# Kernel optimization log

Hardware: AMD Instinct MI355X
Metric: run time of the kernel (lower is better)

The kernel has to match this reference:

```python
import jax, jax.numpy as jnp
import numpy as np
from jax import lax

NUM_HEADS = 8  # init_kwargs: num_heads
TOPK = 7       # hard-coded in DMF.forward


def setup_inputs() -> dict:
    key = jax.random.key(0)
    k1, k2, k3, k4 = jax.random.split(key, 4)
    b, dim, H, W = 8, 384, 128, 128
    x = jax.random.normal(k1, (b, dim, H, W), dtype=jnp.float32)
    qkv_w = jax.random.normal(k2, (dim * 3, dim), dtype=jnp.float32) * 0.05   # 1x1 conv weight
    dw_w = jax.random.normal(k3, (dim * 3, 1, 3, 3), dtype=jnp.float32) * 0.05  # depthwise 3x3
    proj_w = jax.random.normal(k4, (dim, dim), dtype=jnp.float32) * 0.05     # 1x1 conv weight
    temperature = jnp.ones((NUM_HEADS, 1, 1), dtype=jnp.float32)
    return {"x": x, "qkv_w": qkv_w, "dw_w": dw_w, "proj_w": proj_w, "temperature": temperature}


def _l2norm(t, eps=1e-12):
    # matches torch.nn.functional.normalize(dim=-1)
    n = jnp.sqrt(jnp.sum(t * t, axis=-1, keepdims=True))
    return t / jnp.maximum(n, eps)


def reference(x, qkv_w, dw_w, proj_w, temperature):
    b, c, h, w = x.shape
    ch = c // NUM_HEADS  # channels per head

    # 1x1 conv (pointwise) -> depthwise 3x3 conv
    qkv = jnp.einsum('bchw,oc->bohw', x, qkv_w)
    qkv = lax.conv_general_dilated(
        qkv, dw_w, window_strides=(1, 1), padding=[(1, 1), (1, 1)],
        feature_group_count=qkv.shape[1],
        dimension_numbers=('NCHW', 'OIHW', 'NCHW'))
    q, k, v = jnp.split(qkv, 3, axis=1)

    def to_heads(t):  # b (head ch) h w -> b head ch (h w)
        return t.reshape(b, NUM_HEADS, ch, h * w)

    q = _l2norm(to_heads(q))
    k = _l2norm(to_heads(k))
    v = to_heads(v)

    # channel attention: [b, head, ch, ch]
    attn_weight = jnp.einsum('bhcn,bhdn->bhcd', q, k) * temperature

    # top-k sparsify along last dim, then masked softmax
    _, idx = lax.top_k(attn_weight, TOPK)                      # [b,h,ch,TOPK]
    cols = jnp.arange(attn_weight.shape[-1])
    mask = (idx[..., None] == cols).any(axis=-2)               # [b,h,ch,ch] bool
    attn = jnp.where(mask, attn_weight, -jnp.inf)
    attn = jax.nn.softmax(attn, axis=-1)

    out = jnp.einsum('bhcd,bhdn->bhcn', attn, v).reshape(b, c, h, w)
    out = jnp.einsum('bchw,oc->bohw', out, proj_w)
    return out
```

## Files before the change

kernel.cpp:

```cpp
#include <hip/hip_runtime.h>

#define HWN 16384
#define WDIM 128

typedef __bf16 bf16x8 __attribute__((ext_vector_type(8)));
typedef float floatx4 __attribute__((ext_vector_type(4)));

#define LSTR 36

__global__ __launch_bounds__(256, 2) void gemm_mfma3(
    const __bf16* __restrict__ Ah, const __bf16* __restrict__ Al,
    const float* __restrict__ B, float* __restrict__ C,
    int K, long sA, long sB, long sC) {
  __shared__ __bf16 sAh[128 * LSTR], sAl[128 * LSTR], sBh[128 * LSTR], sBl[128 * LSTR];
  const int bz = blockIdx.z;
  Ah += (long)bz * sA;
  Al += (long)bz * sA;
  B += (long)bz * sB;
  C += (long)bz * sC;
  const int tid = threadIdx.x;
  const int n0 = blockIdx.x << 7, m0 = blockIdx.y << 7;
  const int arow = tid >> 1, akq = (tid & 1) << 4;
  const int bn = (tid & 63) << 1;
  const int bkb = (tid >> 6) << 3;
  const int lane = tid & 63, wv = tid >> 6;
  const int mq = (wv & 1) << 6, nq = (wv >> 1) << 6;
  const int fm = lane & 15, fq = lane >> 4;
  floatx4 acc[4][4] = {};
  for (int k0 = 0; k0 < K; k0 += 32) {
    const __bf16* pAh = Ah + (long)(m0 + arow) * K + k0 + akq;
    const __bf16* pAl = Al + (long)(m0 + arow) * K + k0 + akq;
    bf16x8 a0 = *(const bf16x8*)pAh;
    bf16x8 a1 = *(const bf16x8*)(pAh + 8);
    bf16x8 a2 = *(const bf16x8*)pAl;
    bf16x8 a3 = *(const bf16x8*)(pAl + 8);
    const float* pB = B + (long)(k0 + bkb) * HWN + n0 + bn;
    float2 v[8];
#pragma unroll
    for (int r = 0; r < 8; ++r) v[r] = *(const float2*)(pB + (long)r * HWN);
    bf16x8 bh0, bh1, bl0, bl1;
#pragma unroll
    for (int r = 0; r < 8; ++r) {
      float vx = v[r].x, vy = v[r].y;
      __bf16 hx = (__bf16)vx, hy = (__bf16)vy;
      bh0[r] = hx;
      bh1[r] = hy;
      bl0[r] = (__bf16)(vx - (float)hx);
      bl1[r] = (__bf16)(vy - (float)hy);
    }
    __syncthreads();
    *(bf16x8*)&sAh[arow * LSTR + akq] = a0;
    *(bf16x8*)&sAh[arow * LSTR + akq + 8] = a1;
    *(bf16x8*)&sAl[arow * LSTR + akq] = a2;
    *(bf16x8*)&sAl[arow * LSTR + akq + 8] = a3;
    *(bf16x8*)&sBh[bn * LSTR + bkb] = bh0;
    *(bf16x8*)&sBh[(bn + 1) * LSTR + bkb] = bh1;
    *(bf16x8*)&sBl[bn * LSTR + bkb] = bl0;
    *(bf16x8*)&sBl[(bn + 1) * LSTR + bkb] = bl1;
    __syncthreads();
    bf16x8 fAh[4], fAl[4];
#pragma unroll
    for (int i = 0; i < 4; ++i) {
      fAh[i] = *(const bf16x8*)&sAh[(mq + i * 16 + fm) * LSTR + fq * 8];
      fAl[i] = *(const bf16x8*)&sAl[(mq + i * 16 + fm) * LSTR + fq * 8];
    }
#pragma unroll
    for (int j = 0; j < 4; ++j) {
      bf16x8 bh = *(const bf16x8*)&sBh[(nq + j * 16 + fm) * LSTR + fq * 8];
      bf16x8 bl = *(const bf16x8*)&sBl[(nq + j * 16 + fm) * LSTR + fq * 8];
#pragma unroll
      for (int i = 0; i < 4; ++i) {
        acc[i][j] = __builtin_amdgcn_mfma_f32_16x16x32_bf16(fAh[i], bh, acc[i][j], 0, 0, 0);
        acc[i][j] = __builtin_amdgcn_mfma_f32_16x16x32_bf16(fAl[i], bh, acc[i][j], 0, 0, 0);
        acc[i][j] = __builtin_amdgcn_mfma_f32_16x16x32_bf16(fAh[i], bl, acc[i][j], 0, 0, 0);
      }
    }
  }
#pragma unroll
  for (int i = 0; i < 4; ++i)
#pragma unroll
    for (int j = 0; j < 4; ++j) {
      const int col = n0 + nq + j * 16 + fm;
#pragma unroll
      for (int r = 0; r < 4; ++r) {
        const int row = m0 + mq + i * 16 + fq * 4 + r;
        C[(long)row * HWN + col] = acc[i][j][r];
      }
    }
}

__global__ __launch_bounds__(256) void split_w(
    const float* __restrict__ w, __bf16* __restrict__ hi, __bf16* __restrict__ lo, int n) {
  int i = blockIdx.x * 256 + threadIdx.x;
  if (i < n) {
    float v = w[i];
    __bf16 h = (__bf16)v;
    hi[i] = h;
    lo[i] = (__bf16)(v - (float)h);
  }
}

__global__ __launch_bounds__(256) void dw_all3(
    const float* __restrict__ qkv1, const float* __restrict__ dww,
    float* __restrict__ dwout, float* __restrict__ qs, float* __restrict__ ks, int b0) {
  const int tid = threadIdx.x;
  const int ch = blockIdx.x;
  const int yh = blockIdx.y;
  const int bz = blockIdx.z;
  const int xg = tid & 31;
  const int rg = tid >> 5;
  const float4* P = (const float4*)(qkv1 + ((long)bz * 1152 + ch) * HWN);
  float4* O = (float4*)(dwout + ((long)bz * 1152 + ch) * HWN);
  const float* wp = dww + (long)ch * 9;
  const float w00 = wp[0], w01 = wp[1], w02 = wp[2];
  const float w10 = wp[3], w11 = wp[4], w12 = wp[5];
  const float w20 = wp[6], w21 = wp[7], w22 = wp[8];
  const int y0 = (yh << 6) + (rg << 3);

  float4 vr[10];
#pragma unroll
  for (int r = 0; r < 10; ++r) {
    int yy = y0 - 1 + r;
    vr[r] = make_float4(0.f, 0.f, 0.f, 0.f);
    if (yy >= 0 && yy < WDIM) vr[r] = P[yy * 32 + xg];
  }
  float lf[10], rt[10];
#pragma unroll
  for (int r = 0; r < 10; ++r) {
    float l_ = __shfl_up(vr[r].w, 1, 64);
    float r_ = __shfl_down(vr[r].x, 1, 64);
    lf[r] = (xg == 0) ? 0.f : l_;
    rt[r] = (xg == 31) ? 0.f : r_;
  }
  float sq = 0.f;
#pragma unroll
  for (int i = 0; i < 8; ++i) {
    const float t0 = lf[i], t1 = vr[i].x, t2 = vr[i].y, t3 = vr[i].z, t4 = vr[i].w, t5 = rt[i];
    const float m0_ = lf[i + 1], m1 = vr[i + 1].x, m2 = vr[i + 1].y, m3 = vr[i + 1].z,
                m4 = vr[i + 1].w, m5 = rt[i + 1];
    const float b0_ = lf[i + 2], b1 = vr[i + 2].x, b2 = vr[i + 2].y, b3 = vr[i + 2].z,
                b4 = vr[i + 2].w, b5 = rt[i + 2];
    float o0 = w00 * t0 + w01 * t1 + w02 * t2 + w10 * m0_ + w11 * m1 + w12 * m2 +
               w20 * b0_ + w21 * b1 + w22 * b2;
    float o1 = w00 * t1 + w01 * t2 + w02 * t3 + w10 * m1 + w11 * m2 + w12 * m3 +
               w20 * b1 + w21 * b2 + w22 * b3;
    float o2 = w00 * t2 + w01 * t3 + w02 * t4 + w10 * m2 + w11 * m3 + w12 * m4 +
               w20 * b2 + w21 * b3 + w22 * b4;
    float o3 = w00 * t3 + w01 * t4 + w02 * t5 + w10 * m3 + w11 * m4 + w12 * m5 +
               w20 * b3 + w21 * b4 + w22 * b5;
    sq += o0 * o0 + o1 * o1 + o2 * o2 + o3 * o3;
    O[(y0 + i) * 32 + xg] = make_float4(o0, o1, o2, o3);
  }

  if (ch < 768) {
#pragma unroll
    for (int off = 32; off >= 1; off >>= 1) sq += __shfl_down(sq, off, 64);
    if ((tid & 63) == 0) {
      int b = b0 + bz;
      if (ch < 384)
        atomicAdd(qs + b * 384 + ch, sq);
      else
        atomicAdd(ks + b * 384 + (ch - 384), sq);
    }
  }
}

#define GPAD 132
__global__ __launch_bounds__(256) void gram256(
    const float* __restrict__ dwout, float* __restrict__ gram, int b0) {
  __shared__ float qt[48 * GPAD];
  __shared__ float kt[48 * GPAD];
  const int tid = threadIdx.x;
  const int kc = blockIdx.x;
  const int h = blockIdx.y;
  const int bz = blockIdx.z;
  const float* Q = dwout + ((long)bz * 1152 + h * 48) * HWN;
  const float* K = Q + 384L * HWN;
  const int c0 = (tid & 15) * 3;
  const int d0 = (tid >> 4) * 3;
  float g[3][3] = {};
  for (int p0 = kc * 512; p0 < kc * 512 + 512; p0 += 128) {
    __syncthreads();
#pragma unroll
    for (int i = tid; i < 1536; i += 256) {
      int r = i >> 5, x4 = (i & 31) << 2;
      *(float4*)&qt[r * GPAD + x4] = *(const float4*)(Q + (long)r * HWN + p0 + x4);
      *(float4*)&kt[r * GPAD + x4] = *(const float4*)(K + (long)r * HWN + p0 + x4);
    }
    __syncthreads();
#pragma unroll 4
    for (int p = 0; p < 128; p += 4) {
      float4 qv[3], kv[3];
#pragma unroll
      for (int i = 0; i < 3; ++i) qv[i] = *(const float4*)&qt[(c0 + i) * GPAD + p];
#pragma unroll
      for (int j = 0; j < 3; ++j) kv[j] = *(const float4*)&kt[(d0 + j) * GPAD + p];
#pragma unroll
      for (int i = 0; i < 3; ++i)
#pragma unroll
        for (int j = 0; j < 3; ++j)
          g[i][j] += qv[i].x * kv[j].x + qv[i].y * kv[j].y + qv[i].z * kv[j].z +
                     qv[i].w * kv[j].w;
    }
  }
  float* gb = gram + (long)((b0 + bz) * 8 + h) * 2304;
#pragma unroll
  for (int i = 0; i < 3; ++i)
#pragma unroll
    for (int j = 0; j < 3; ++j) atomicAdd(gb + (c0 + i) * 48 + (d0 + j), g[i][j]);
}

__global__ __launch_bounds__(64) void topk_softmax(
    const float* __restrict__ gram, const float* __restrict__ qs, const float* __restrict__ ks,
    const float* __restrict__ temp, float* __restrict__ attn, int b0) {
  const int z = blockIdx.x;
  const int b = b0 + (z >> 3), h = z & 7;
  __shared__ float kn[48];
  const int tid = threadIdx.x;
  if (tid < 48) kn[tid] = fmaxf(sqrtf(ks[b * 384 + h * 48 + tid]), 1e-12f);
  __syncthreads();
  if (tid >= 48) return;
  const int c = tid;
  float qn = fmaxf(sqrtf(qs[b * 384 + h * 48 + c]), 1e-12f);
  float tv = temp[h];
  const float* gr = gram + (long)(b * 8 + h) * 2304 + c * 48;
  float s[48];
#pragma unroll
  for (int d = 0; d < 48; ++d) s[d] = gr[d] / (qn * kn[d]) * tv;
  unsigned long long sel = 0ull;
  float m0 = 0.f;
  for (int it = 0; it < 7; ++it) {
    float mx = -3.0e38f;
    int mi = 0;
#pragma unroll
    for (int d = 0; d < 48; ++d) {
      bool taken = (sel >> d) & 1ull;
      if (!taken && s[d] > mx) { mx = s[d]; mi = d; }
    }
    sel |= (1ull << mi);
    if (it == 0) m0 = mx;
  }
  float sum = 0.f;
  float e[48];
#pragma unroll
  for (int d = 0; d < 48; ++d) {
    bool t = (sel >> d) & 1ull;
    float ev = t ? expf(s[d] - m0) : 0.f;
    e[d] = ev;
    sum += ev;
  }
  float inv = 1.f / sum;
  float* ar = attn + (long)(b * 8 + h) * 2304 + c * 48;
#pragma unroll
  for (int d = 0; d < 48; ++d) ar[d] = e[d] * inv;
}

__global__ __launch_bounds__(256) void build_M(
    const float* __restrict__ attn, const float* __restrict__ pw,
    __bf16* __restrict__ Mh, __bf16* __restrict__ Ml, int b0) {
  const int b = b0 + blockIdx.x;
  const int h = blockIdx.y;
  __shared__ float at[48][49];
  const int tid = threadIdx.x;
  for (int i = tid; i < 2304; i += 256) at[i / 48][i % 48] = attn[(long)(b * 8 + h) * 2304 + i];
  __syncthreads();
  for (int idx = tid; idx < 384 * 48; idx += 256) {
    int o = idx / 48, d = idx % 48;
    const float* pr = pw + (long)o * 384 + h * 48;
    float acc = 0.f;
#pragma unroll
    for (int c = 0; c < 48; ++c) acc += pr[c] * at[c][d];
    long oi = ((long)b * 384 + o) * 384 + h * 48 + d;
    __bf16 hh = (__bf16)acc;
    Mh[oi] = hh;
    Ml[oi] = (__bf16)(acc - (float)hh);
  }
}

extern "C" void kernel_launch(void* const* d_in, const int* in_sizes, int n_in,
                              void* d_out, int out_size, void* d_ws, size_t ws_size,
                              hipStream_t stream) {
  const float* x = (const float*)d_in[0];
  const float* qkv_w = (const float*)d_in[1];
  const float* dw_w = (const float*)d_in[2];
  const float* proj_w = (const float*)d_in[3];
  const float* temp = (const float*)d_in[4];
  float* out = (float*)d_out;
  float* ws = (float*)d_ws;

  float* gram = ws;
  float* qs = gram + 147456;
  float* ks = qs + 3072;
  float* attn = ks + 3072;
  __bf16* Wh = (__bf16*)(attn + 147456);
  __bf16* Wl = Wh + 442368;
  __bf16* Mh = Wl + 442368;
  __bf16* Ml = Mh + 1179648;
  float* qkv1 = (float*)(Ml + 1179648);
  const long SMALLS = 1333248L;
  const long PERB = 37748736L;
  long wsf = (long)(ws_size / 4);
  int nb = (int)((wsf - SMALLS) / PERB);
  if (nb < 1) nb = 1;
  if (nb > 8) nb = 8;
  float* dwout = qkv1 + (long)nb * 18874368L;

  hipMemsetAsync(gram, 0, (147456 + 3072 + 3072) * sizeof(float), stream);
  split_w<<<dim3((442368 + 255) / 256), 256, 0, stream>>>(qkv_w, Wh, Wl, 442368);

  for (int b0 = 0; b0 < 8; b0 += nb) {
    int nbc = (8 - b0 < nb) ? (8 - b0) : nb;
    gemm_mfma3<<<dim3(128, 9, nbc), 256, 0, stream>>>(
        Wh, Wl, x + (long)b0 * 6291456L, qkv1, 384, 0L, 6291456L, 18874368L);
    dw_all3<<<dim3(1152, 2, nbc), 256, 0, stream>>>(qkv1, dw_w, dwout, qs, ks, b0);
    gram256<<<dim3(32, 8, nbc), 256, 0, stream>>>(dwout, gram, b0);
    topk_softmax<<<dim3(nbc * 8), 64, 0, stream>>>(gram, qs, ks, temp, attn, b0);
    build_M<<<dim3(nbc, 8), 256, 0, stream>>>(attn, proj_w, Mh, Ml, b0);
    gemm_mfma3<<<dim3(128, 3, nbc), 256, 0, stream>>>(
        Mh + (long)b0 * 147456L, Ml + (long)b0 * 147456L, dwout + 768L * HWN,
        out + (long)b0 * 6291456L, 384, 147456L, 18874368L, 6291456L);
  }
}
```

Before: 1.412 ms.

## Fuse depthwise conv into gram kernel, store V as split bf16, merge topk with M

The q/k depthwise convolution is now recomputed inside the gram kernel, one image row at a time into shared memory, so the fp32 q/k dwout tensors are never written or read back. A separate kernel applies the conv only to the v channels and stores them pre-split into bf16 hi/lo halves. The final GEMM then reads bf16 B operands directly instead of converting fp32 on load. topk_softmax and build_M are merged into one kernel, and the workspace per batch shrinks so more batches fit per chunk. The cost is extra per-row loads and conv arithmetic inside the gram kernel, plus a gram grid that now loops over rows of the image.

After: 1.679 ms. 18.9% more time.

```diff
diff --git a/kernel.cpp b/kernel.cpp
--- a/kernel.cpp
+++ b/kernel.cpp
@@ -4,6 +4,8 @@
 #define WDIM 128
 
 typedef __bf16 bf16x8 __attribute__((ext_vector_type(8)));
+typedef __bf16 bf16x4 __attribute__((ext_vector_type(4)));
+typedef __bf16 bf16x2 __attribute__((ext_vector_type(2)));
 typedef float floatx4 __attribute__((ext_vector_type(4)));
 
 #define LSTR 36
@@ -89,6 +91,90 @@
     }
 }
 
+__global__ __launch_bounds__(256, 2) void gemm_bf3(
+    const __bf16* __restrict__ Ah, const __bf16* __restrict__ Al,
+    const __bf16* __restrict__ Bh, const __bf16* __restrict__ Bl,
+    float* __restrict__ C, int K, long sA, long sB, long sC) {
+  __shared__ __bf16 sAh[128 * LSTR], sAl[128 * LSTR], sBh[128 * LSTR], sBl[128 * LSTR];
+  const int bz = blockIdx.z;
+  Ah += (long)bz * sA;
+  Al += (long)bz * sA;
+  Bh += (long)bz * sB;
+  Bl += (long)bz * sB;
+  C += (long)bz * sC;
+  const int tid = threadIdx.x;
+  const int n0 = blockIdx.x << 7, m0 = blockIdx.y << 7;
+  const int arow = tid >> 1, akq = (tid & 1) << 4;
+  const int bn = (tid & 63) << 1;
+  const int bkb = (tid >> 6) << 3;
+  const int lane = tid & 63, wv = tid >> 6;
+  const int mq = (wv & 1) << 6, nq = (wv >> 1) << 6;
+  const int fm = lane & 15, fq = lane >> 4;
+  floatx4 acc[4][4] = {};
+  for (int k0 = 0; k0 < K; k0 += 32) {
+    const __bf16* pAh = Ah + (long)(m0 + arow) * K + k0 + akq;
+    const __bf16* pAl = Al + (long)(m0 + arow) * K + k0 + akq;
+    bf16x8 a0 = *(const bf16x8*)pAh;
+    bf16x8 a1 = *(const bf16x8*)(pAh + 8);
+    bf16x8 a2 = *(const bf16x8*)pAl;
+    bf16x8 a3 = *(const bf16x8*)(pAl + 8);
+    const __bf16* pBh = Bh + (long)(k0 + bkb) * HWN + n0 + bn;
+    const __bf16* pBl = Bl + (long)(k0 + bkb) * HWN + n0 + bn;
+    bf16x2 vh[8], vl[8];
+#pragma unroll
+    for (int r = 0; r < 8; ++r) {
+      vh[r] = *(const bf16x2*)(pBh + (long)r * HWN);
+      vl[r] = *(const bf16x2*)(pBl + (long)r * HWN);
+    }
+    bf16x8 bh0, bh1, bl0, bl1;
+#pragma unroll
+    for (int r = 0; r < 8; ++r) {
+      bh0[r] = vh[r][0];
+      bh1[r] = vh[r][1];
+      bl0[r] = vl[r][0];
+      bl1[r] = vl[r][1];
+    }
+    __syncthreads();
+    *(bf16x8*)&sAh[arow * LSTR + akq] = a0;
+    *(bf16x8*)&sAh[arow * LSTR + akq + 8] = a1;
+    *(bf16x8*)&sAl[arow * LSTR + akq] = a2;
+    *(bf16x8*)&sAl[arow * LSTR + akq + 8] = a3;
+    *(bf16x8*)&sBh[bn * LSTR + bkb] = bh0;
+    *(bf16x8*)&sBh[(bn + 1) * LSTR + bkb] = bh1;
+    *(bf16x8*)&sBl[bn * LSTR + bkb] = bl0;
+    *(bf16x8*)&sBl[(bn + 1) * LSTR + bkb] = bl1;
+    __syncthreads();
+    bf16x8 fAh[4], fAl[4];
+#pragma unroll
+    for (int i = 0; i < 4; ++i) {
+      fAh[i] = *(const bf16x8*)&sAh[(mq + i * 16 + fm) * LSTR + fq * 8];
+      fAl[i] = *(const bf16x8*)&sAl[(mq + i * 16 + fm) * LSTR + fq * 8];
+    }
+#pragma unroll
+    for (int j = 0; j < 4; ++j) {
+      bf16x8 bh = *(const bf16x8*)&sBh[(nq + j * 16 + fm) * LSTR + fq * 8];
+      bf16x8 bl = *(const bf16x8*)&sBl[(nq + j * 16 + fm) * LSTR + fq * 8];
+#pragma unroll
+      for (int i = 0; i < 4; ++i) {
+        acc[i][j] = __builtin_amdgcn_mfma_f32_16x16x32_bf16(fAh[i], bh, acc[i][j], 0, 0, 0);
+        acc[i][j] = __builtin_amdgcn_mfma_f32_16x16x32_bf16(fAl[i], bh, acc[i][j], 0, 0, 0);
+        acc[i][j] = __builtin_amdgcn_mfma_f32_16x16x32_bf16(fAh[i], bl, acc[i][j], 0, 0, 0);
+      }
+    }
+  }
+#pragma unroll
+  for (int i = 0; i < 4; ++i)
+#pragma unroll
+    for (int j = 0; j < 4; ++j) {
+      const int col = n0 + nq + j * 16 + fm;
+#pragma unroll
+      for (int r = 0; r < 4; ++r) {
+        const int row = m0 + mq + i * 16 + fq * 4 + r;
+        C[(long)row * HWN + col] = acc[i][j][r];
+      }
+    }
+}
+
 __global__ __launch_bounds__(256) void split_w(
     const float* __restrict__ w, __bf16* __restrict__ hi, __bf16* __restrict__ lo, int n) {
   int i = blockIdx.x * 256 + threadIdx.x;
@@ -100,23 +186,21 @@
   }
 }
 
-__global__ __launch_bounds__(256) void dw_all3(
+__global__ __launch_bounds__(256) void dw_v(
     const float* __restrict__ qkv1, const float* __restrict__ dww,
-    float* __restrict__ dwout, float* __restrict__ qs, float* __restrict__ ks, int b0) {
+    __bf16* __restrict__ Vh, __bf16* __restrict__ Vl) {
   const int tid = threadIdx.x;
   const int ch = blockIdx.x;
   const int yh = blockIdx.y;
   const int bz = blockIdx.z;
   const int xg = tid & 31;
   const int rg = tid >> 5;
-  const float4* P = (const float4*)(qkv1 + ((long)bz * 1152 + ch) * HWN);
-  float4* O = (float4*)(dwout + ((long)bz * 1152 + ch) * HWN);
-  const float* wp = dww + (long)ch * 9;
+  const float4* P = (const float4*)(qkv1 + ((long)bz * 1152 + 768 + ch) * HWN);
+  const float* wp = dww + (long)(768 + ch) * 9;
   const float w00 = wp[0], w01 = wp[1], w02 = wp[2];
   const float w10 = wp[3], w11 = wp[4], w12 = wp[5];
   const float w20 = wp[6], w21 = wp[7], w22 = wp[8];
   const int y0 = (yh << 6) + (rg << 3);
-
   float4 vr[10];
 #pragma unroll
   for (int r = 0; r < 10; ++r) {
@@ -132,7 +216,7 @@
     lf[r] = (xg == 0) ? 0.f : l_;
     rt[r] = (xg == 31) ? 0.f : r_;
   }
-  float sq = 0.f;
+  const long obase = ((long)bz * 384 + ch) * HWN;
 #pragma unroll
   for (int i = 0; i < 8; ++i) {
     const float t0 = lf[i], t1 = vr[i].x, t2 = vr[i].y, t3 = vr[i].z, t4 = vr[i].w, t5 = rt[i];
@@ -148,53 +232,79 @@
                w20 * b2 + w21 * b3 + w22 * b4;
     float o3 = w00 * t3 + w01 * t4 + w02 * t5 + w10 * m3 + w11 * m4 + w12 * m5 +
                w20 * b3 + w21 * b4 + w22 * b5;
-    sq += o0 * o0 + o1 * o1 + o2 * o2 + o3 * o3;
-    O[(y0 + i) * 32 + xg] = make_float4(o0, o1, o2, o3);
-  }
-
-  if (ch < 768) {
-#pragma unroll
-    for (int off = 32; off >= 1; off >>= 1) sq += __shfl_down(sq, off, 64);
-    if ((tid & 63) == 0) {
-      int b = b0 + bz;
-      if (ch < 384)
-        atomicAdd(qs + b * 384 + ch, sq);
-      else
-        atomicAdd(ks + b * 384 + (ch - 384), sq);
-    }
+    bf16x4 h4, l4;
+    __bf16 h0 = (__bf16)o0, h1 = (__bf16)o1, h2 = (__bf16)o2, h3 = (__bf16)o3;
+    h4[0] = h0; h4[1] = h1; h4[2] = h2; h4[3] = h3;
+    l4[0] = (__bf16)(o0 - (float)h0);
+    l4[1] = (__bf16)(o1 - (float)h1);
+    l4[2] = (__bf16)(o2 - (float)h2);
+    l4[3] = (__bf16)(o3 - (float)h3);
+    long off = obase + (y0 + i) * WDIM + xg * 4;
+    *(bf16x4*)&Vh[off] = h4;
+    *(bf16x4*)&Vl[off] = l4;
   }
 }
 
 #define GPAD 132
-__global__ __launch_bounds__(256) void gram256(
-    const float* __restrict__ dwout, float* __restrict__ gram, int b0) {
-  __shared__ float qt[48 * GPAD];
-  __shared__ float kt[48 * GPAD];
+__global__ __launch_bounds__(256) void gram_dw(
+    const float* __restrict__ qkv1, const float* __restrict__ dww,
+    float* __restrict__ gram, float* __restrict__ qs, float* __restrict__ ks, int b0) {
+  __shared__ float dq[48 * GPAD];
+  __shared__ float dk[48 * GPAD];
   const int tid = threadIdx.x;
-  const int kc = blockIdx.x;
+  const int yc = blockIdx.x;
   const int h = blockIdx.y;
   const int bz = blockIdx.z;
-  const float* Q = dwout + ((long)bz * 1152 + h * 48) * HWN;
-  const float* K = Q + 384L * HWN;
+  const int xg = tid & 31;
+  const int grp = tid >> 5;
   const int c0 = (tid & 15) * 3;
   const int d0 = (tid >> 4) * 3;
+  const long bb = (long)bz * 1152;
   float g[3][3] = {};
-  for (int p0 = kc * 512; p0 < kc * 512 + 512; p0 += 128) {
-    __syncthreads();
-#pragma unroll
-    for (int i = tid; i < 1536; i += 256) {
-      int r = i >> 5, x4 = (i & 31) << 2;
-      *(float4*)&qt[r * GPAD + x4] = *(const float4*)(Q + (long)r * HWN + p0 + x4);
-      *(float4*)&kt[r * GPAD + x4] = *(const float4*)(K + (long)r * HWN + p0 + x4);
+  float sq[12] = {};
+  for (int y = yc * 4; y < yc * 4 + 4; ++y) {
+    __syncthreads();
+#pragma unroll
+    for (int gi = 0; gi < 12; ++gi) {
+      const int cl = grp * 12 + gi;
+      const int gch = (cl < 48) ? (h * 48 + cl) : (384 + h * 48 + (cl - 48));
+      const float* sp = qkv1 + (bb + gch) * HWN;
+      const float* wp = dww + (long)gch * 9;
+      float4 r0 = make_float4(0.f, 0.f, 0.f, 0.f);
+      float4 r2 = make_float4(0.f, 0.f, 0.f, 0.f);
+      if (y > 0) r0 = *(const float4*)(sp + (y - 1) * WDIM + xg * 4);
+      float4 r1 = *(const float4*)(sp + y * WDIM + xg * 4);
+      if (y < WDIM - 1) r2 = *(const float4*)(sp + (y + 1) * WDIM + xg * 4);
+      float l0 = __shfl_up(r0.w, 1, 32), l1 = __shfl_up(r1.w, 1, 32), l2 = __shfl_up(r2.w, 1, 32);
+      float q0 = __shfl_down(r0.x, 1, 32), q1 = __shfl_down(r1.x, 1, 32),
+            q2 = __shfl_down(r2.x, 1, 32);
+      if (xg == 0) { l0 = 0.f; l1 = 0.f; l2 = 0.f; }
+      if (xg == 31) { q0 = 0.f; q1 = 0.f; q2 = 0.f; }
+      const float w00 = wp[0], w01 = wp[1], w02 = wp[2];
+      const float w10 = wp[3], w11 = wp[4], w12 = wp[5];
+      const float w20 = wp[6], w21 = wp[7], w22 = wp[8];
+      const float e0[6] = {l0, r0.x, r0.y, r0.z, r0.w, q0};
+      const float e1[6] = {l1, r1.x, r1.y, r1.z, r1.w, q1};
+      const float e2[6] = {l2, r2.x, r2.y, r2.z, r2.w, q2};
+      float o[4];
+#pragma unroll
+      for (int j = 0; j < 4; ++j) {
+        o[j] = w00 * e0[j] + w01 * e0[j + 1] + w02 * e0[j + 2] +
+               w10 * e1[j] + w11 * e1[j + 1] + w12 * e1[j + 2] +
+               w20 * e2[j] + w21 * e2[j + 1] + w22 * e2[j + 2];
+        sq[gi] += o[j] * o[j];
+      }
+      float* dst = (cl < 48) ? &dq[cl * GPAD] : &dk[(cl - 48) * GPAD];
+      *(float4*)&dst[xg * 4] = make_float4(o[0], o[1], o[2], o[3]);
     }
     __syncthreads();
 #pragma unroll 4
     for (int p = 0; p < 128; p += 4) {
       float4 qv[3], kv[3];
 #pragma unroll
-      for (int i = 0; i < 3; ++i) qv[i] = *(const float4*)&qt[(c0 + i) * GPAD + p];
-#pragma unroll
-      for (int j = 0; j < 3; ++j) kv[j] = *(const float4*)&kt[(d0 + j) * GPAD + p];
+      for (int i = 0; i < 3; ++i) qv[i] = *(const float4*)&dq[(c0 + i) * GPAD + p];
+#pragma unroll
+      for (int j = 0; j < 3; ++j) kv[j] = *(const float4*)&dk[(d0 + j) * GPAD + p];
 #pragma unroll
       for (int i = 0; i < 3; ++i)
 #pragma unroll
@@ -203,66 +313,72 @@
                      qv[i].w * kv[j].w;
     }
   }
-  float* gb = gram + (long)((b0 + bz) * 8 + h) * 2304;
+  const int b = b0 + bz;
+#pragma unroll
+  for (int gi = 0; gi < 12; ++gi) {
+    float s = sq[gi];
+#pragma unroll
+    for (int off = 16; off >= 1; off >>= 1) s += __shfl_down(s, off, 32);
+    if (xg == 0) {
+      int cl = grp * 12 + gi;
+      if (cl < 48)
+        atomicAdd(qs + b * 384 + h * 48 + cl, s);
+      else
+        atomicAdd(ks + b * 384 + h * 48 + (cl - 48), s);
+    }
+  }
+  float* gb = gram + (long)(b * 8 + h) * 2304;
 #pragma unroll
   for (int i = 0; i < 3; ++i)
 #pragma unroll
     for (int j = 0; j < 3; ++j) atomicAdd(gb + (c0 + i) * 48 + (d0 + j), g[i][j]);
 }
 
-__global__ __launch_bounds__(64) void topk_softmax(
+__global__ __launch_bounds__(256) void attn_M(
     const float* __restrict__ gram, const float* __restrict__ qs, const float* __restrict__ ks,
-    const float* __restrict__ temp, float* __restrict__ attn, int b0) {
+    const float* __restrict__ temp, const float* __restrict__ pw,
+    __bf16* __restrict__ Mh, __bf16* __restrict__ Ml, int b0) {
   const int z = blockIdx.x;
   const int b = b0 + (z >> 3), h = z & 7;
   __shared__ float kn[48];
+  __shared__ float at[48][49];
   const int tid = threadIdx.x;
   if (tid < 48) kn[tid] = fmaxf(sqrtf(ks[b * 384 + h * 48 + tid]), 1e-12f);
   __syncthreads();
-  if (tid >= 48) return;
-  const int c = tid;
-  float qn = fmaxf(sqrtf(qs[b * 384 + h * 48 + c]), 1e-12f);
-  float tv = temp[h];
-  const float* gr = gram + (long)(b * 8 + h) * 2304 + c * 48;
-  float s[48];
-#pragma unroll
-  for (int d = 0; d < 48; ++d) s[d] = gr[d] / (qn * kn[d]) * tv;
-  unsigned long long sel = 0ull;
-  float m0 = 0.f;
-  for (int it = 0; it < 7; ++it) {
-    float mx = -3.0e38f;
-    int mi = 0;
+  if (tid < 48) {
+    const int c = tid;
+    float qn = fmaxf(sqrtf(qs[b * 384 + h * 48 + c]), 1e-12f);
+    float tv = temp[h];
+    const float* gr = gram + (long)(b * 8 + h) * 2304 + c * 48;
+    float s[48];
+#pragma unroll
+    for (int d = 0; d < 48; ++d) s[d] = gr[d] / (qn * kn[d]) * tv;
+    unsigned long long sel = 0ull;
+    float m0 = 0.f;
+    for (int it = 0; it < 7; ++it) {
+      float mx = -3.0e38f;
+      int mi = 0;
+#pragma unroll
+      for (int d = 0; d < 48; ++d) {
+        bool taken = (sel >> d) & 1ull;
+        if (!taken && s[d] > mx) { mx = s[d]; mi = d; }
+      }
+      sel |= (1ull << mi);
+      if (it == 0) m0 = mx;
+    }
+    float sum = 0.f;
+    float e[48];
 #pragma unroll
     for (int d = 0; d < 48; ++d) {
-      bool taken = (sel >> d) & 1ull;
-      if (!taken && s[d] > mx) { mx = s[d]; mi = d; }
-    }
-    sel |= (1ull << mi);
-    if (it == 0) m0 = mx;
-  }
-  float sum = 0.f;
-  float e[48];
-#pragma unroll
-  for (int d = 0; d < 48; ++d) {
-    bool t = (sel >> d) & 1ull;
-    float ev = t ? expf(s[d] - m0) : 0.f;
-    e[d] = ev;
-    sum += ev;
-  }
-  float inv = 1.f / sum;
-  float* ar = attn + (long)(b * 8 + h) * 2304 + c * 48;
-#pragma unroll
-  for (int d = 0; d < 48; ++d) ar[d] = e[d] * inv;
-}
-
-__global__ __launch_bounds__(256) void build_M(
-    const float* __restrict__ attn, const float* __restrict__ pw,
-    __bf16* __restrict__ Mh, __bf16* __restrict__ Ml, int b0) {
-  const int b = b0 + blockIdx.x;
-  const int h = blockIdx.y;
-  __shared__ float at[48][49];
-  const int tid = threadIdx.x;
-  for (int i = tid; i < 2304; i += 256) at[i / 48][i % 48] = attn[(long)(b * 8 + h) * 2304 + i];
+      bool t = (sel >> d) & 1ull;
+      float ev = t ? expf(s[d] - m0) : 0.f;
+      e[d] = ev;
+      sum += ev;
+    }
+    float inv = 1.f / sum;
+#pragma unroll
+    for (int d = 0; d < 48; ++d) at[c][d] = e[d] * inv;
+  }
   __syncthreads();
   for (int idx = tid; idx < 384 * 48; idx += 256) {
     int o = idx / 48, d = idx % 48;
@@ -291,19 +407,19 @@
   float* gram = ws;
   float* qs = gram + 147456;
   float* ks = qs + 3072;
-  float* attn = ks + 3072;
-  __bf16* Wh = (__bf16*)(attn + 147456);
+  __bf16* Wh = (__bf16*)(ks + 3072);
   __bf16* Wl = Wh + 442368;
   __bf16* Mh = Wl + 442368;
   __bf16* Ml = Mh + 1179648;
   float* qkv1 = (float*)(Ml + 1179648);
-  const long SMALLS = 1333248L;
-  const long PERB = 37748736L;
+  const long SMALLS = 1775616L;
+  const long PERB = 25165824L;
   long wsf = (long)(ws_size / 4);
   int nb = (int)((wsf - SMALLS) / PERB);
   if (nb < 1) nb = 1;
   if (nb > 8) nb = 8;
-  float* dwout = qkv1 + (long)nb * 18874368L;
+  __bf16* Vh = (__bf16*)(qkv1 + (long)nb * 18874368L);
+  __bf16* Vl = Vh + (long)nb * 6291456L;
 
   hipMemsetAsync(gram, 0, (147456 + 3072 + 3072) * sizeof(float), stream);
   split_w<<<dim3((442368 + 255) / 256), 256, 0, stream>>>(qkv_w, Wh, Wl, 442368);
@@ -312,12 +428,11 @@
     int nbc = (8 - b0 < nb) ? (8 - b0) : nb;
     gemm_mfma3<<<dim3(128, 9, nbc), 256, 0, stream>>>(
         Wh, Wl, x + (long)b0 * 6291456L, qkv1, 384, 0L, 6291456L, 18874368L);
-    dw_all3<<<dim3(1152, 2, nbc), 256, 0, stream>>>(qkv1, dw_w, dwout, qs, ks, b0);
-    gram256<<<dim3(32, 8, nbc), 256, 0, stream>>>(dwout, gram, b0);
-    topk_softmax<<<dim3(nbc * 8), 64, 0, stream>>>(gram, qs, ks, temp, attn, b0);
-    build_M<<<dim3(nbc, 8), 256, 0, stream>>>(attn, proj_w, Mh, Ml, b0);
-    gemm_mfma3<<<dim3(128, 3, nbc), 256, 0, stream>>>(
-        Mh + (long)b0 * 147456L, Ml + (long)b0 * 147456L, dwout + 768L * HWN,
-        out + (long)b0 * 6291456L, 384, 147456L, 18874368L, 6291456L);
-  }
-}
+    dw_v<<<dim3(384, 2, nbc), 256, 0, stream>>>(qkv1, dw_w, Vh, Vl);
+    gram_dw<<<dim3(32, 8, nbc), 256, 0, stream>>>(qkv1, dw_w, gram, qs, ks, b0);
+    attn_M<<<dim3(nbc * 8), 256, 0, stream>>>(gram, qs, ks, temp, proj_w, Mh, Ml, b0);
+    gemm_bf3<<<dim3(128, 3, nbc), 256, 0, stream>>>(
+        Mh + (long)b0 * 147456L, Ml + (long)b0 * 147456L, Vh, Vl,
+        out + (long)b0 * 6291456L, 384, 147456L, 6291456L, 6291456L);
+  }
+}
```
